# Optimization experiments

Measured on AMD Instinct MI355X. Metric: run time of the kernel, lower is better.

Reference implementation:

```python
import jax, jax.numpy as jnp
import numpy as np


def setup_inputs() -> dict:
    key = jax.random.key(0)
    k1, k2 = jax.random.split(key)
    B, C, H, W = 16, 128, 32, 32   # C == embedding_dim
    K = 2048                        # codebook size (num_embeddings)
    x = jax.random.normal(k1, (B, C, H, W), dtype=jnp.float32)
    codebook = jax.random.normal(k2, (K, C), dtype=jnp.float32)
    return {"x": x, "codebook": codebook}


def reference(x, codebook):
    # x: [B, C, H, W] -> NHWC -> flatten to [N, C]
    B, C, H, W = x.shape
    x_nhwc = jnp.transpose(x, (0, 2, 3, 1))
    x_flat = x_nhwc.reshape(-1, C)                      # [N, C]
    # Squared L2 distances via expansion (argmin-equivalent to torch.norm
    # of the broadcast difference, without the [N, K, C] intermediate):
    x_sq = jnp.sum(x_flat * x_flat, axis=1, keepdims=True)   # [N, 1]
    w_sq = jnp.sum(codebook * codebook, axis=1)              # [K]
    d2 = x_sq - 2.0 * (x_flat @ codebook.T) + w_sq           # [N, K]
    encoding_indices = jnp.argmin(d2, axis=1)                # [N]
    encodings = jax.nn.one_hot(encoding_indices, codebook.shape[0],
                               dtype=x_flat.dtype)           # [N, K]
    quantized = encodings @ codebook                         # [N, C]
    quantized = jnp.transpose(quantized.reshape(B, H, W, C), (0, 3, 1, 2))
    return encodings, quantized
```

## Files before the change

### kernel.cpp

```cpp
#include <hip/hip_runtime.h>
#include <hip/hip_bf16.h>

#define N_TOK  16384
#define KCODES 2048
#define CDIM   128
#define BM     64
#define TPB    512
#define NTILE  16
#define CAP    40
#define DELTA  5.0f
#define ASTR   68

typedef __attribute__((ext_vector_type(8))) short bhalf8;
typedef __attribute__((ext_vector_type(4))) float facc4;

__global__ __launch_bounds__(256) void prep_kernel(const float* __restrict__ cb,
                                                   bhalf8* __restrict__ cbt,
                                                   float* __restrict__ wsq) {
    const int T   = blockIdx.x;
    const int tid = threadIdx.x;
    const int r   = tid >> 4;
    const int g   = tid & 15;
    const float4* src = (const float4*)(cb + ((size_t)(T * 16 + r)) * CDIM + g * 8);
    float4 a0 = src[0], a1 = src[1];

    float s = a0.x*a0.x + a0.y*a0.y + a0.z*a0.z + a0.w*a0.w
            + a1.x*a1.x + a1.y*a1.y + a1.z*a1.z + a1.w*a1.w;
    s += __shfl_xor(s, 1, 64);
    s += __shfl_xor(s, 2, 64);
    s += __shfl_xor(s, 4, 64);
    s += __shfl_xor(s, 8, 64);
    if (g == 0) wsq[T * 16 + r] = s;

    union { unsigned u[4]; bhalf8 v; } fu;
    __hip_bfloat162 h0 = __float22bfloat162_rn(make_float2(a0.x, a0.y));
    __hip_bfloat162 h1 = __float22bfloat162_rn(make_float2(a0.z, a0.w));
    __hip_bfloat162 h2 = __float22bfloat162_rn(make_float2(a1.x, a1.y));
    __hip_bfloat162 h3 = __float22bfloat162_rn(make_float2(a1.z, a1.w));
    fu.u[0] = *(unsigned*)&h0; fu.u[1] = *(unsigned*)&h1;
    fu.u[2] = *(unsigned*)&h2; fu.u[3] = *(unsigned*)&h3;
    const int kf = g >> 2, q = g & 3;
    cbt[(size_t)T * 256 + kf * 64 + q * 16 + r] = fu.v;
}

__global__ __launch_bounds__(TPB, 2) void argmin_kernel(const float* __restrict__ x,
                                                        const float* __restrict__ cb,
                                                        const bhalf8* __restrict__ cbt,
                                                        const float* __restrict__ wsqg,
                                                        float* __restrict__ enc,
                                                        float* __restrict__ quant) {
    __shared__ float As[CDIM][ASTR];
    __shared__ float wsqs[KCODES];
    __shared__ float redvw[8][BM];
    __shared__ float rowthr[BM];
    __shared__ int   cnt[BM];
    __shared__ int   candk[BM][CAP];
    __shared__ int   rowidx[BM];

    const int tid  = threadIdx.x;
    const int lane = tid & 63;
    const int w    = tid >> 6;
    const int q    = lane >> 4;
    const int r    = lane & 15;
    const int n0   = blockIdx.x * BM;
    const int b    = n0 >> 10;
    const int hw0  = n0 & 1023;
    const int cbase = w * 256;
    const size_t zb = (size_t)n0 * KCODES;
    const float4 z4 = {0.f, 0.f, 0.f, 0.f};

    {
        int m4 = (tid & 15) << 2;
        int c0 = tid >> 4;
        #pragma unroll
        for (int i = 0; i < 4; i++) {
            int c = c0 + 32 * i;
            float4 v = *(const float4*)(x + (((size_t)(b * CDIM + c)) << 10) + hw0 + m4);
            *(float4*)(&As[c][m4]) = v;
        }
    }
    #pragma unroll
    for (int i = 0; i < KCODES / TPB; i++) wsqs[i * TPB + tid] = wsqg[i * TPB + tid];
    if (tid < BM) cnt[tid] = 0;
    __syncthreads();

    bhalf8 af[4][4];
    #pragma unroll
    for (int rt = 0; rt < 4; rt++) {
        int m = rt * 16 + r;
        #pragma unroll
        for (int kf = 0; kf < 4; kf++) {
            union { unsigned u[4]; bhalf8 v; } fu;
            #pragma unroll
            for (int p = 0; p < 4; p++) {
                int k = kf * 32 + q * 8 + 2 * p;
                __hip_bfloat162 h = __float22bfloat162_rn(make_float2(As[k][m], As[k + 1][m]));
                fu.u[p] = *(unsigned*)&h;
            }
            af[rt][kf] = fu.v;
        }
    }

    float rmin[16];
    #pragma unroll
    for (int t = 0; t < 16; t++) rmin[t] = 3.0e38f;

    {
        bhalf8 bf[4];
        #pragma unroll
        for (int kf = 0; kf < 4; kf++)
            bf[kf] = cbt[((size_t)(cbase >> 4)) * 256 + kf * 64 + lane];
        #pragma unroll
        for (int t = 0; t < NTILE; t++) {
            bhalf8 bn[4];
            if (t + 1 < NTILE) {
                size_t tb = ((size_t)((cbase >> 4) + t + 1)) * 256;
                #pragma unroll
                for (int kf = 0; kf < 4; kf++) bn[kf] = cbt[tb + kf * 64 + lane];
            }
            facc4 acc[4];
            #pragma unroll
            for (int rt = 0; rt < 4; rt++) acc[rt] = (facc4){0.f, 0.f, 0.f, 0.f};
            #pragma unroll
            for (int kf = 0; kf < 4; kf++)
                #pragma unroll
                for (int rt = 0; rt < 4; rt++)
                    acc[rt] = __builtin_amdgcn_mfma_f32_16x16x32_bf16(af[rt][kf], bf[kf], acc[rt], 0, 0, 0);
            float wv = wsqs[cbase + t * 16 + r];
            #pragma unroll
            for (int rt = 0; rt < 4; rt++)
                #pragma unroll
                for (int i = 0; i < 4; i++)
                    rmin[rt * 4 + i] = fminf(rmin[rt * 4 + i], fmaf(-2.f, acc[rt][i], wv));
            int j0 = t * 2;
            *(float4*)(enc + zb + (size_t)(j0 * TPB + tid) * 4) = z4;
            *(float4*)(enc + zb + (size_t)((j0 + 1) * TPB + tid) * 4) = z4;
            if (t + 1 < NTILE) {
                #pragma unroll
                for (int kf = 0; kf < 4; kf++) bf[kf] = bn[kf];
            }
        }
    }

    #pragma unroll
    for (int t = 0; t < 16; t++) {
        float v = rmin[t];
        v = fminf(v, __shfl_xor(v, 1, 64));
        v = fminf(v, __shfl_xor(v, 2, 64));
        v = fminf(v, __shfl_xor(v, 4, 64));
        v = fminf(v, __shfl_xor(v, 8, 64));
        if (r == 0) redvw[w][(t >> 2) * 16 + q * 4 + (t & 3)] = v;
    }
    __syncthreads();
    if (tid < BM) {
        float mv = redvw[0][tid];
        #pragma unroll
        for (int i = 1; i < 8; i++) mv = fminf(mv, redvw[i][tid]);
        rowthr[tid] = mv + DELTA;
    }
    __syncthreads();

    float thr[16];
    #pragma unroll
    for (int t = 0; t < 16; t++) thr[t] = rowthr[(t >> 2) * 16 + q * 4 + (t & 3)];

    {
        bhalf8 bf[4];
        #pragma unroll
        for (int kf = 0; kf < 4; kf++)
            bf[kf] = cbt[((size_t)(cbase >> 4)) * 256 + kf * 64 + lane];
        #pragma unroll
        for (int t = 0; t < NTILE; t++) {
            bhalf8 bn[4];
            if (t + 1 < NTILE) {
                size_t tb = ((size_t)((cbase >> 4) + t + 1)) * 256;
                #pragma unroll
                for (int kf = 0; kf < 4; kf++) bn[kf] = cbt[tb + kf * 64 + lane];
            }
            facc4 acc[4];
            #pragma unroll
            for (int rt = 0; rt < 4; rt++) acc[rt] = (facc4){0.f, 0.f, 0.f, 0.f};
            #pragma unroll
            for (int kf = 0; kf < 4; kf++)
                #pragma unroll
                for (int rt = 0; rt < 4; rt++)
                    acc[rt] = __builtin_amdgcn_mfma_f32_16x16x32_bf16(af[rt][kf], bf[kf], acc[rt], 0, 0, 0);
            float wv = wsqs[cbase + t * 16 + r];
            #pragma unroll
            for (int rt = 0; rt < 4; rt++)
                #pragma unroll
                for (int i = 0; i < 4; i++) {
                    float d = fmaf(-2.f, acc[rt][i], wv);
                    if (d <= thr[rt * 4 + i]) {
                        int row = rt * 16 + q * 4 + i;
                        int p = atomicAdd(&cnt[row], 1);
                        if (p < CAP) candk[row][p] = cbase + t * 16 + r;
                    }
                }
            int j0 = 32 + t * 2;
            *(float4*)(enc + zb + (size_t)(j0 * TPB + tid) * 4) = z4;
            *(float4*)(enc + zb + (size_t)((j0 + 1) * TPB + tid) * 4) = z4;
            if (t + 1 < NTILE) {
                #pragma unroll
                for (int kf = 0; kf < 4; kf++) bf[kf] = bn[kf];
            }
        }
    }
    __syncthreads();

    for (int m = 8 * w; m < 8 * w + 8; m++) {
        int c = min(cnt[m], CAP);
        float bv = 3.0e38f; int bk = 0x7fffffff;
        for (int t = 0; t < c; t++) {
            int k = candk[m][t];
            float x0 = As[lane][m], x1 = As[lane + 64][m];
            float c0 = cb[(size_t)k * CDIM + lane];
            float c1 = cb[(size_t)k * CDIM + 64 + lane];
            float s = x0 * c0 + x1 * c1;
            #pragma unroll
            for (int off = 1; off <= 32; off <<= 1) s += __shfl_xor(s, off, 64);
            float d = fmaf(-2.f, s, wsqs[k]);
            if (d < bv || (d == bv && k < bk)) { bv = d; bk = k; }
        }
        if (lane == 0) rowidx[m] = bk;
    }
    __syncthreads();

    if (tid < BM) enc[(size_t)(n0 + tid) * KCODES + rowidx[tid]] = 1.0f;

    #pragma unroll
    for (int i = tid; i < BM * CDIM / 4; i += TPB) {
        int c  = i >> 4;
        int hq = (i & 15) << 2;
        float4 v;
        v.x = cb[(size_t)rowidx[hq + 0] * CDIM + c];
        v.y = cb[(size_t)rowidx[hq + 1] * CDIM + c];
        v.z = cb[(size_t)rowidx[hq + 2] * CDIM + c];
        v.w = cb[(size_t)rowidx[hq + 3] * CDIM + c];
        *(float4*)(quant + (((size_t)(b * CDIM + c)) << 10) + hw0 + hq) = v;
    }
}

extern "C" void kernel_launch(void* const* d_in, const int* in_sizes, int n_in,
                              void* d_out, int out_size, void* d_ws, size_t ws_size,
                              hipStream_t stream) {
    const float* x  = (const float*)d_in[0];
    const float* cb = (const float*)d_in[1];
    float* out = (float*)d_out;

    bhalf8* cbt  = (bhalf8*)d_ws;
    float*  wsqp = (float*)((char*)d_ws + 512 * 1024);

    prep_kernel<<<KCODES / 16, 256, 0, stream>>>(cb, cbt, wsqp);
    argmin_kernel<<<N_TOK / BM, TPB, 0, stream>>>(x, cb, cbt, wsqp,
                                                  out, out + (size_t)N_TOK * KCODES);
}
```

Before: 203.0 us.

## Specialize warps: four compute codebook slices, four stream zero-fill of encodings

```diff
diff --git a/kernel.cpp b/kernel.cpp
--- a/kernel.cpp
+++ b/kernel.cpp
@@ -6,7 +6,9 @@
 #define CDIM   128
 #define BM     64
 #define TPB    512
-#define NTILE  16
+#define NCW    4
+#define CPW    (KCODES / NCW)
+#define TPW    (CPW / 16)
 #define CAP    40
 #define DELTA  5.0f
 #define ASTR   68
@@ -43,7 +45,7 @@
     cbt[(size_t)T * 256 + kf * 64 + q * 16 + r] = fu.v;
 }
 
-__global__ __launch_bounds__(TPB, 2) void argmin_kernel(const float* __restrict__ x,
+__global__ __launch_bounds__(TPB, 1) void argmin_kernel(const float* __restrict__ x,
                                                         const float* __restrict__ cb,
                                                         const bhalf8* __restrict__ cbt,
                                                         const float* __restrict__ wsqg,
@@ -51,7 +53,7 @@
                                                         float* __restrict__ quant) {
     __shared__ float As[CDIM][ASTR];
     __shared__ float wsqs[KCODES];
-    __shared__ float redvw[8][BM];
+    __shared__ float redvw[NCW][BM];
     __shared__ float rowthr[BM];
     __shared__ int   cnt[BM];
     __shared__ int   candk[BM][CAP];
@@ -65,8 +67,6 @@
     const int n0   = blockIdx.x * BM;
     const int b    = n0 >> 10;
     const int hw0  = n0 & 1023;
-    const int cbase = w * 256;
-    const size_t zb = (size_t)n0 * KCODES;
     const float4 z4 = {0.f, 0.f, 0.f, 0.f};
 
     {
@@ -85,38 +85,44 @@
     __syncthreads();
 
     bhalf8 af[4][4];
-    #pragma unroll
-    for (int rt = 0; rt < 4; rt++) {
-        int m = rt * 16 + r;
-        #pragma unroll
-        for (int kf = 0; kf < 4; kf++) {
-            union { unsigned u[4]; bhalf8 v; } fu;
-            #pragma unroll
-            for (int p = 0; p < 4; p++) {
-                int k = kf * 32 + q * 8 + 2 * p;
-                __hip_bfloat162 h = __float22bfloat162_rn(make_float2(As[k][m], As[k + 1][m]));
-                fu.u[p] = *(unsigned*)&h;
+    if (w < NCW) {
+        #pragma unroll
+        for (int rt = 0; rt < 4; rt++) {
+            int m = rt * 16 + r;
+            #pragma unroll
+            for (int kf = 0; kf < 4; kf++) {
+                union { unsigned u[4]; bhalf8 v; } fu;
+                #pragma unroll
+                for (int p = 0; p < 4; p++) {
+                    int k = kf * 32 + q * 8 + 2 * p;
+                    __hip_bfloat162 h = __float22bfloat162_rn(make_float2(As[k][m], As[k + 1][m]));
+                    fu.u[p] = *(unsigned*)&h;
+                }
+                af[rt][kf] = fu.v;
             }
-            af[rt][kf] = fu.v;
-        }
-    }
-
-    float rmin[16];
-    #pragma unroll
-    for (int t = 0; t < 16; t++) rmin[t] = 3.0e38f;
-
-    {
-        bhalf8 bf[4];
-        #pragma unroll
-        for (int kf = 0; kf < 4; kf++)
-            bf[kf] = cbt[((size_t)(cbase >> 4)) * 256 + kf * 64 + lane];
-        #pragma unroll
-        for (int t = 0; t < NTILE; t++) {
-            bhalf8 bn[4];
-            if (t + 1 < NTILE) {
-                size_t tb = ((size_t)((cbase >> 4) + t + 1)) * 256;
-                #pragma unroll
-                for (int kf = 0; kf < 4; kf++) bn[kf] = cbt[tb + kf * 64 + lane];
+        }
+    }
+
+    const int    cw  = w * CPW;
+    const size_t tb0 = (size_t)(cw >> 4) * 256;
+
+    if (w < NCW) {
+        float rmin[16];
+        #pragma unroll
+        for (int t = 0; t < 16; t++) rmin[t] = 3.0e38f;
+
+        bhalf8 bcur[4], bnxt[4];
+        #pragma unroll
+        for (int kf = 0; kf < 4; kf++) bcur[kf] = cbt[tb0 + kf * 64 + lane];
+        #pragma unroll
+        for (int kf = 0; kf < 4; kf++) bnxt[kf] = cbt[tb0 + 256 + kf * 64 + lane];
+
+        for (int t = 0; t < TPW; t++) {
+            bhalf8 bn2[4];
+            if (t + 2 < TPW) {
+                size_t tb = tb0 + (size_t)(t + 2) * 256;
+                #pragma unroll
+                for (int kf = 0; kf < 4; kf++) bn2[kf] = cbt[tb + kf * 64 + lane];
             }
             facc4 acc[4];
             #pragma unroll
@@ -125,57 +131,56 @@
             for (int kf = 0; kf < 4; kf++)
                 #pragma unroll
                 for (int rt = 0; rt < 4; rt++)
-                    acc[rt] = __builtin_amdgcn_mfma_f32_16x16x32_bf16(af[rt][kf], bf[kf], acc[rt], 0, 0, 0);
-            float wv = wsqs[cbase + t * 16 + r];
+                    acc[rt] = __builtin_amdgcn_mfma_f32_16x16x32_bf16(af[rt][kf], bcur[kf], acc[rt], 0, 0, 0);
+            float wv = wsqs[cw + t * 16 + r];
             #pragma unroll
             for (int rt = 0; rt < 4; rt++)
                 #pragma unroll
                 for (int i = 0; i < 4; i++)
                     rmin[rt * 4 + i] = fminf(rmin[rt * 4 + i], fmaf(-2.f, acc[rt][i], wv));
-            int j0 = t * 2;
-            *(float4*)(enc + zb + (size_t)(j0 * TPB + tid) * 4) = z4;
-            *(float4*)(enc + zb + (size_t)((j0 + 1) * TPB + tid) * 4) = z4;
-            if (t + 1 < NTILE) {
-                #pragma unroll
-                for (int kf = 0; kf < 4; kf++) bf[kf] = bn[kf];
-            }
-        }
-    }
-
-    #pragma unroll
-    for (int t = 0; t < 16; t++) {
-        float v = rmin[t];
-        v = fminf(v, __shfl_xor(v, 1, 64));
-        v = fminf(v, __shfl_xor(v, 2, 64));
-        v = fminf(v, __shfl_xor(v, 4, 64));
-        v = fminf(v, __shfl_xor(v, 8, 64));
-        if (r == 0) redvw[w][(t >> 2) * 16 + q * 4 + (t & 3)] = v;
+            #pragma unroll
+            for (int kf = 0; kf < 4; kf++) { bcur[kf] = bnxt[kf]; bnxt[kf] = bn2[kf]; }
+        }
+        #pragma unroll
+        for (int t = 0; t < 16; t++) {
+            float v = rmin[t];
+            v = fminf(v, __shfl_xor(v, 1, 64));
+            v = fminf(v, __shfl_xor(v, 2, 64));
+            v = fminf(v, __shfl_xor(v, 4, 64));
+            v = fminf(v, __shfl_xor(v, 8, 64));
+            if (r == 0) redvw[w][(t >> 2) * 16 + q * 4 + (t & 3)] = v;
+        }
+    } else {
+        const int f = w - NCW;
+        float4* dst = (float4*)(enc + (size_t)(n0 + f * 16) * KCODES);
+        #pragma unroll 8
+        for (int i = 0; i < 64; i++) dst[(size_t)i * 64 + lane] = z4;
     }
     __syncthreads();
     if (tid < BM) {
-        float mv = redvw[0][tid];
-        #pragma unroll
-        for (int i = 1; i < 8; i++) mv = fminf(mv, redvw[i][tid]);
+        float mv = fminf(fminf(redvw[0][tid], redvw[1][tid]),
+                         fminf(redvw[2][tid], redvw[3][tid]));
         rowthr[tid] = mv + DELTA;
     }
     __syncthreads();
 
-    float thr[16];
-    #pragma unroll
-    for (int t = 0; t < 16; t++) thr[t] = rowthr[(t >> 2) * 16 + q * 4 + (t & 3)];
-
-    {
-        bhalf8 bf[4];
-        #pragma unroll
-        for (int kf = 0; kf < 4; kf++)
-            bf[kf] = cbt[((size_t)(cbase >> 4)) * 256 + kf * 64 + lane];
-        #pragma unroll
-        for (int t = 0; t < NTILE; t++) {
-            bhalf8 bn[4];
-            if (t + 1 < NTILE) {
-                size_t tb = ((size_t)((cbase >> 4) + t + 1)) * 256;
-                #pragma unroll
-                for (int kf = 0; kf < 4; kf++) bn[kf] = cbt[tb + kf * 64 + lane];
+    if (w < NCW) {
+        float thr[16];
+        #pragma unroll
+        for (int t = 0; t < 16; t++) thr[t] = rowthr[(t >> 2) * 16 + q * 4 + (t & 3)];
+
+        bhalf8 bcur[4], bnxt[4];
+        #pragma unroll
+        for (int kf = 0; kf < 4; kf++) bcur[kf] = cbt[tb0 + kf * 64 + lane];
+        #pragma unroll
+        for (int kf = 0; kf < 4; kf++) bnxt[kf] = cbt[tb0 + 256 + kf * 64 + lane];
+
+        for (int t = 0; t < TPW; t++) {
+            bhalf8 bn2[4];
+            if (t + 2 < TPW) {
+                size_t tb = tb0 + (size_t)(t + 2) * 256;
+                #pragma unroll
+                for (int kf = 0; kf < 4; kf++) bn2[kf] = cbt[tb + kf * 64 + lane];
             }
             facc4 acc[4];
             #pragma unroll
@@ -184,8 +189,8 @@
             for (int kf = 0; kf < 4; kf++)
                 #pragma unroll
                 for (int rt = 0; rt < 4; rt++)
-                    acc[rt] = __builtin_amdgcn_mfma_f32_16x16x32_bf16(af[rt][kf], bf[kf], acc[rt], 0, 0, 0);
-            float wv = wsqs[cbase + t * 16 + r];
+                    acc[rt] = __builtin_amdgcn_mfma_f32_16x16x32_bf16(af[rt][kf], bcur[kf], acc[rt], 0, 0, 0);
+            float wv = wsqs[cw + t * 16 + r];
             #pragma unroll
             for (int rt = 0; rt < 4; rt++)
                 #pragma unroll
@@ -194,17 +199,17 @@
                     if (d <= thr[rt * 4 + i]) {
                         int row = rt * 16 + q * 4 + i;
                         int p = atomicAdd(&cnt[row], 1);
-                        if (p < CAP) candk[row][p] = cbase + t * 16 + r;
+                        if (p < CAP) candk[row][p] = cw + t * 16 + r;
                     }
                 }
-            int j0 = 32 + t * 2;
-            *(float4*)(enc + zb + (size_t)(j0 * TPB + tid) * 4) = z4;
-            *(float4*)(enc + zb + (size_t)((j0 + 1) * TPB + tid) * 4) = z4;
-            if (t + 1 < NTILE) {
-                #pragma unroll
-                for (int kf = 0; kf < 4; kf++) bf[kf] = bn[kf];
-            }
-        }
+            #pragma unroll
+            for (int kf = 0; kf < 4; kf++) { bcur[kf] = bnxt[kf]; bnxt[kf] = bn2[kf]; }
+        }
+    } else {
+        const int f = w - NCW;
+        float4* dst = (float4*)(enc + (size_t)(n0 + f * 16) * KCODES);
+        #pragma unroll 8
+        for (int i = 64; i < 128; i++) dst[(size_t)i * 64 + lane] = z4;
     }
     __syncthreads();
 
```

Measured after the change: 191.3 us. 5.8% less time.
